# Optimization experiments

Measured on AMD Instinct MI355X. Metric: run time of the kernel, lower is better.

The kernel has to match this reference:

```python
import jax, jax.numpy as jnp
import numpy as np
import itertools

EPSILON = 1e-6
OUT_SIZE = 4096
IN_SIZE = 4096
RANK = 2  # in_rank + len(out_shape)
REGION = np.array([16.0, 16.0], dtype=np.float32)
PRIMES = np.array([2, 3], dtype=np.int64)  # first RANK primes from the buffer
# floor/ceil combinations, same order as itertools.product([True, False], repeat=RANK)
FLOOR_MASK = np.array([[int(b) for b in bools] for bools in itertools.product([True, False], repeat=RANK)], dtype=bool)  # (2**RANK, RANK)


def generate_integer_tuples(means, rr_u, g_u, rng_sizes, region):
    # means: (b, k, RANK); rr_u/g_u: uniform(0,1) samples (b, k, radd/gadd, RANK)
    b, k, rank = means.shape
    m = jax.lax.stop_gradient(means)  # torch uses means.data
    mexp = m[:, :, None, :]
    # all floor/ceil corner combinations of the continuous index tuple
    neigh = jnp.where(FLOOR_MASK[None, None, :, :], jnp.floor(mexp), jnp.ceil(mexp)).astype(jnp.int64)
    # uniform samples over the whole index space
    g_ints = jnp.floor(g_u * (1.0 - EPSILON) * rng_sizes).astype(jnp.int64)
    # uniform samples from a small window around round(means)
    mr = jnp.round(mexp)
    lower = mr - region * 0.5
    upper = mr + region * 0.5
    lower = jnp.where(lower < 0.0, 0.0, lower)
    lower = jnp.where(upper > rng_sizes, rng_sizes - region, lower)
    rr_ints = (rr_u * (1.0 - EPSILON) * region + lower).astype(jnp.int64)
    ints = jnp.concatenate([neigh, g_ints, rr_ints], axis=2)  # (b, k, 2**RANK+gadd+radd, RANK)
    return ints.reshape(b, -1, rank)


def duplicates(tuples):
    # tuples: (b, n, r) int64 -> bool mask (b, n) marking all-but-first occurrences
    b, n, r = tuples.shape
    unique = jnp.prod((tuples + 1) ** PRIMES[:r], axis=2)  # prime-power hash
    sort_idx = jnp.argsort(unique, axis=1)
    sorted_v = jnp.take_along_axis(unique, sort_idx, axis=1)
    unsort_idx = jnp.argsort(sort_idx, axis=1)
    mask = jnp.concatenate(
        [jnp.zeros((b, 1), dtype=bool), sorted_v[:, 1:] == sorted_v[:, :-1]], axis=1)
    return jnp.take_along_axis(mask, unsort_idx, axis=1)


def densities(points, means, sigmas):
    # unnormalized diagonal-MVN pdf: exp(-0.5 * sum_r (p_r - m_r)^2 / (eps + sigma_r))
    # expanded quadratic form via einsum to avoid the (b, n, k, r) intermediate
    inv = 1.0 / (EPSILON + sigmas)                                   # (b, k, r)
    a = jnp.einsum('bnr,bkr->bnk', points * points, inv)
    bt = jnp.einsum('bnr,bkr->bnk', points, means * inv)
    c = jnp.sum(means * means * inv, axis=-1)[:, None, :]
    return jnp.exp(-0.5 * (a - 2.0 * bt + c))                        # (b, n, k)


def setup_inputs() -> dict:
    key = jax.random.key(0)
    ks = jax.random.split(key, 7)
    b, k, gadd, radd = 4, 256, 64, 64
    rng = jnp.array([OUT_SIZE, IN_SIZE], dtype=jnp.float32)
    x = jax.random.normal(ks[0], (b, IN_SIZE), dtype=jnp.float32)
    means = jax.random.uniform(ks[1], (b, k, RANK), dtype=jnp.float32) * (rng - 1.0)
    sigmas = (jax.random.uniform(ks[2], (b, k, RANK), dtype=jnp.float32) * 2.0 + 0.5) * (rng / 64.0)
    values = jax.random.normal(ks[3], (b, k), dtype=jnp.float32)
    bias = jax.random.normal(ks[4], (OUT_SIZE,), dtype=jnp.float32)
    rr_u = jax.random.uniform(ks[5], (b, k, radd, RANK), dtype=jnp.float32)
    g_u = jax.random.uniform(ks[6], (b, k, gadd, RANK), dtype=jnp.float32)
    return {"x": x, "means": means, "sigmas": sigmas, "values": values,
            "bias": bias, "rr_u": rr_u, "g_u": g_u}


def reference(x, means, sigmas, values, bias, rr_u, g_u):
    b, in_size = x.shape
    rng_sizes = jnp.array([OUT_SIZE, in_size], dtype=jnp.float32)
    region = jnp.asarray(REGION)
    indices = jax.lax.stop_gradient(
        generate_integer_tuples(means, rr_u, g_u, rng_sizes, region))  # (b, n, 2)
    dups = duplicates(indices)                                        # (b, n) bool
    props = densities(indices.astype(jnp.float32), means, sigmas)     # (b, n, k)
    props = jnp.where(dups[:, :, None], 0.0, props)                   # zero duplicates
    props = props / props.sum(axis=1, keepdims=True)
    weights = jnp.einsum('bnk,bk->bn', props, values)                 # per-index weight
    out_idx = indices[:, :, 0]  # output coordinate (len(out_shape)=1)
    in_idx = indices[:, :, 1]   # input coordinate (in_rank=1)
    gathered = jnp.take_along_axis(x, in_idx, axis=1)                 # (b, n)
    barange = jnp.arange(b)[:, None]
    y = jnp.zeros((b, OUT_SIZE), dtype=x.dtype).at[barange, out_idx].add(weights * gathered)
    return y + bias[None, :]
```

## Files before the change

### kernel.cpp

```cpp
#include <hip/hip_runtime.h>
#include <cstdint>

#define BATCH 4
#define KCOMP 256
#define GADD 64
#define RADD 64
#define PPK 132
#define NPB (KCOMP * PPK)
#define NTOT (BATCH * NPB)
#define OUTS 4096
#define INS 4096
#define TBITS 16
#define TSIZE (1 << TBITS)
#define TILE 128
#define TILES (NPB / TILE)

#define KEYS_BYTES  ((size_t)BATCH * TSIZE * 8)
#define DENOM_BYTES ((size_t)BATCH * KCOMP * 4)
#define VALS_BYTES  ((size_t)BATCH * TSIZE * 4)
#define PTS_BYTES   ((size_t)NTOT * 4)

#define ZERO_U4 131328
#define FF_U4   65536
#define Y_F4    4096
#define INIT_TOT (ZERO_U4 + FF_U4 + Y_F4)

__device__ __forceinline__ unsigned long long point_hash(long long t0, long long t1) {
    unsigned long long a = (unsigned long long)((t0 + 1) * (t0 + 1));
    unsigned long long b = (unsigned long long)((t1 + 1) * (t1 + 1) * (t1 + 1));
    return a * b;
}

__device__ __forceinline__ unsigned int slot_of(unsigned long long h) {
    return (unsigned int)((h * 0x9E3779B97F4A7C15ull) >> (64 - TBITS));
}

__global__ void k_init(const float* __restrict__ bias, float* __restrict__ y,
                       uint4* __restrict__ zero_base, uint4* __restrict__ ff_base) {
    int i = blockIdx.x * blockDim.x + threadIdx.x;
    if (i < ZERO_U4) {
        zero_base[i] = make_uint4(0u, 0u, 0u, 0u);
    } else if (i < ZERO_U4 + FF_U4) {
        ff_base[i - ZERO_U4] = make_uint4(~0u, ~0u, ~0u, ~0u);
    } else if (i < INIT_TOT) {
        int j = i - (ZERO_U4 + FF_U4);
        float4 bv = ((const float4*)bias)[j & 1023];
        ((float4*)y)[j] = bv;
    }
}

__global__ void k_gen(const float* __restrict__ means,
                      const float* __restrict__ rr_u,
                      const float* __restrict__ g_u,
                      uint32_t* __restrict__ pts,
                      unsigned long long* __restrict__ keys,
                      unsigned int* __restrict__ vals) {
    int i = blockIdx.x * blockDim.x + threadIdx.x;
    int bk, j;
    long long t0, t1;
    if (i < 4096) {
        bk = i >> 2;
        j = i & 3;
        double m0 = (double)means[bk * 2], m1 = (double)means[bk * 2 + 1];
        t0 = (long long)((j < 2) ? floor(m0) : ceil(m0));
        t1 = (long long)(((j & 1) == 0) ? floor(m1) : ceil(m1));
    } else if (i < 4096 + 65536) {
        int i2 = i - 4096;
        bk = i2 >> 6;
        j = 4 + (i2 & 63);
        const float* gp = g_u + (size_t)i2 * 2;
        t0 = (long long)floor((double)gp[0] * (1.0 - 1e-6) * 4096.0);
        t1 = (long long)floor((double)gp[1] * (1.0 - 1e-6) * 4096.0);
    } else {
        int i3 = i - (4096 + 65536);
        bk = i3 >> 6;
        j = 68 + (i3 & 63);
        const float* rp = rr_u + (size_t)i3 * 2;
        double m0 = (double)means[bk * 2], m1 = (double)means[bk * 2 + 1];
        double mr0 = rint(m0), mr1 = rint(m1);
        double lo0 = mr0 - 8.0;
        if (lo0 < 0.0) lo0 = 0.0;
        if (mr0 + 8.0 > 4096.0) lo0 = 4080.0;
        double lo1 = mr1 - 8.0;
        if (lo1 < 0.0) lo1 = 0.0;
        if (mr1 + 8.0 > 4096.0) lo1 = 4080.0;
        t0 = (long long)((double)rp[0] * (1.0 - 1e-6) * 16.0 + lo0);
        t1 = (long long)((double)rp[1] * (1.0 - 1e-6) * 16.0 + lo1);
    }
    int b = bk >> 8;
    int loc = (bk & 255) * PPK + j;

    pts[(size_t)b * NPB + loc] = (uint32_t)t0 | ((uint32_t)t1 << 12);

    unsigned long long h = point_hash(t0, t1);
    unsigned long long* kb = keys + (size_t)b * TSIZE;
    unsigned int* vb = vals + (size_t)b * TSIZE;
    unsigned int s = slot_of(h);
    for (;;) {
        unsigned long long prev = atomicCAS(&kb[s], 0ull, h);
        if (prev == 0ull || prev == h) {
            atomicMin(&vb[s], (unsigned int)loc);
            break;
        }
        s = (s + 1) & (TSIZE - 1);
    }
}

__global__ void k_denomA(const float* __restrict__ means,
                         const float* __restrict__ sigmas,
                         uint32_t* __restrict__ pts,
                         const unsigned long long* __restrict__ keys,
                         const unsigned int* __restrict__ vals,
                         float* __restrict__ denom) {
    __shared__ float2 spt[TILE];
    int bid = blockIdx.x;
    int b = bid / TILES;
    int tile = bid - b * TILES;
    int t = threadIdx.x;

    if (t < TILE) {
        int loc = tile * TILE + t;
        uint32_t p = pts[(size_t)b * NPB + loc];
        long long t0 = (long long)(p & 0xFFFu);
        long long t1 = (long long)((p >> 12) & 0xFFFu);
        unsigned long long h = point_hash(t0, t1);
        const unsigned long long* kb = keys + (size_t)b * TSIZE;
        const unsigned int* vb = vals + (size_t)b * TSIZE;
        unsigned int s = slot_of(h);
        while (kb[s] != h) s = (s + 1) & (TSIZE - 1);
        if (vb[s] != (unsigned int)loc) {
            pts[(size_t)b * NPB + loc] = p | 0x80000000u;
            spt[t] = make_float2(1.0e9f, 0.0f);
        } else {
            spt[t] = make_float2((float)t0, (float)t1);
        }
    }
    __syncthreads();

    int bk = b * KCOMP + t;
    float m0 = means[bk * 2], m1 = means[bk * 2 + 1];
    float i0 = -0.5f / (1e-6f + sigmas[bk * 2]);
    float i1 = -0.5f / (1e-6f + sigmas[bk * 2 + 1]);

    float a0 = 0.f, a1 = 0.f, a2 = 0.f, a3 = 0.f, a4 = 0.f, a5 = 0.f, a6 = 0.f, a7 = 0.f;
#pragma unroll 4
    for (int j = 0; j < TILE; j += 8) {
        float2 q0 = spt[j],     q1 = spt[j + 1], q2 = spt[j + 2], q3 = spt[j + 3];
        float2 q4 = spt[j + 4], q5 = spt[j + 5], q6 = spt[j + 6], q7 = spt[j + 7];
        float dx, dy;
        dx = q0.x - m0; dy = q0.y - m1; a0 += __expf(dx * dx * i0 + dy * dy * i1);
        dx = q1.x - m0; dy = q1.y - m1; a1 += __expf(dx * dx * i0 + dy * dy * i1);
        dx = q2.x - m0; dy = q2.y - m1; a2 += __expf(dx * dx * i0 + dy * dy * i1);
        dx = q3.x - m0; dy = q3.y - m1; a3 += __expf(dx * dx * i0 + dy * dy * i1);
        dx = q4.x - m0; dy = q4.y - m1; a4 += __expf(dx * dx * i0 + dy * dy * i1);
        dx = q5.x - m0; dy = q5.y - m1; a5 += __expf(dx * dx * i0 + dy * dy * i1);
        dx = q6.x - m0; dy = q6.y - m1; a6 += __expf(dx * dx * i0 + dy * dy * i1);
        dx = q7.x - m0; dy = q7.y - m1; a7 += __expf(dx * dx * i0 + dy * dy * i1);
    }
    atomicAdd(&denom[bk], ((a0 + a1) + (a2 + a3)) + ((a4 + a5) + (a6 + a7)));
}

__global__ void k_scatterB(const float* __restrict__ means,
                           const float* __restrict__ sigmas,
                           const float* __restrict__ values,
                           const float* __restrict__ denom,
                           const float* __restrict__ x,
                           const uint32_t* __restrict__ pts,
                           float* __restrict__ y) {
    __shared__ float4 prm[KCOMP];
    __shared__ float cf[KCOMP];
    __shared__ float wpart[TILE];
    int bid = blockIdx.x;
    int b = bid / TILES;
    int tile = bid - b * TILES;
    int t = threadIdx.x;

    {
        int bk = b * KCOMP + t;
        float i0 = -0.5f / (1e-6f + sigmas[bk * 2]);
        float i1 = -0.5f / (1e-6f + sigmas[bk * 2 + 1]);
        prm[t] = make_float4(means[bk * 2], means[bk * 2 + 1], i0, i1);
        cf[t] = values[bk] / denom[bk];
    }
    __syncthreads();

    int pt_i = t & (TILE - 1);
    int kbase = (t >> 7) * 128;
    int loc = tile * TILE + pt_i;
    uint32_t p = pts[(size_t)b * NPB + loc];
    bool live = !(p & 0x80000000u);

    float w = 0.0f;
    if (live) {
        float p0 = (float)(p & 0xFFFu);
        float p1 = (float)((p >> 12) & 0xFFFu);
        float w0 = 0.f, w1 = 0.f, w2 = 0.f, w3 = 0.f, w4 = 0.f, w5 = 0.f, w6 = 0.f, w7 = 0.f;
#pragma unroll 4
        for (int q = kbase; q < kbase + 128; q += 8) {
            float4 r0 = prm[q],     r1 = prm[q + 1], r2 = prm[q + 2], r3 = prm[q + 3];
            float4 r4 = prm[q + 4], r5 = prm[q + 5], r6 = prm[q + 6], r7 = prm[q + 7];
            float dx, dy;
            dx = p0 - r0.x; dy = p1 - r0.y;
            w0 = fmaf(__expf(dx * dx * r0.z + dy * dy * r0.w), cf[q],     w0);
            dx = p0 - r1.x; dy = p1 - r1.y;
            w1 = fmaf(__expf(dx * dx * r1.z + dy * dy * r1.w), cf[q + 1], w1);
            dx = p0 - r2.x; dy = p1 - r2.y;
            w2 = fmaf(__expf(dx * dx * r2.z + dy * dy * r2.w), cf[q + 2], w2);
            dx = p0 - r3.x; dy = p1 - r3.y;
            w3 = fmaf(__expf(dx * dx * r3.z + dy * dy * r3.w), cf[q + 3], w3);
            dx = p0 - r4.x; dy = p1 - r4.y;
            w4 = fmaf(__expf(dx * dx * r4.z + dy * dy * r4.w), cf[q + 4], w4);
            dx = p0 - r5.x; dy = p1 - r5.y;
            w5 = fmaf(__expf(dx * dx * r5.z + dy * dy * r5.w), cf[q + 5], w5);
            dx = p0 - r6.x; dy = p1 - r6.y;
            w6 = fmaf(__expf(dx * dx * r6.z + dy * dy * r6.w), cf[q + 6], w6);
            dx = p0 - r7.x; dy = p1 - r7.y;
            w7 = fmaf(__expf(dx * dx * r7.z + dy * dy * r7.w), cf[q + 7], w7);
        }
        w = ((w0 + w1) + (w2 + w3)) + ((w4 + w5) + (w6 + w7));
    }
    if (t >= TILE) wpart[pt_i] = w;
    __syncthreads();
    if (t < TILE && live) {
        w += wpart[pt_i];
        int out_idx = (int)(p & 0xFFFu);
        int in_idx = (int)((p >> 12) & 0xFFFu);
        atomicAdd(&y[(size_t)b * OUTS + out_idx], w * x[(size_t)b * INS + in_idx]);
    }
}

extern "C" void kernel_launch(void* const* d_in, const int* in_sizes, int n_in,
                              void* d_out, int out_size, void* d_ws, size_t ws_size,
                              hipStream_t stream) {
    const float* x      = (const float*)d_in[0];
    const float* means  = (const float*)d_in[1];
    const float* sigmas = (const float*)d_in[2];
    const float* values = (const float*)d_in[3];
    const float* bias   = (const float*)d_in[4];
    const float* rr_u   = (const float*)d_in[5];
    const float* g_u    = (const float*)d_in[6];
    float* y = (float*)d_out;

    uint8_t* w = (uint8_t*)d_ws;
    unsigned long long* keys = (unsigned long long*)w;
    float* denom = (float*)(w + KEYS_BYTES);
    unsigned int* vals = (unsigned int*)(w + KEYS_BYTES + DENOM_BYTES);
    uint32_t* pts = (uint32_t*)(w + KEYS_BYTES + DENOM_BYTES + VALS_BYTES);

    hipLaunchKernelGGL(k_init, dim3((INIT_TOT + 255) / 256), dim3(256), 0, stream,
                       bias, y, (uint4*)w, (uint4*)(w + KEYS_BYTES + DENOM_BYTES));
    hipLaunchKernelGGL(k_gen, dim3((NTOT + 255) / 256), dim3(256), 0, stream,
                       means, rr_u, g_u, pts, keys, vals);
    hipLaunchKernelGGL(k_denomA, dim3(BATCH * TILES), dim3(256), 0, stream,
                       means, sigmas, pts, keys, vals, denom);
    hipLaunchKernelGGL(k_scatterB, dim3(BATCH * TILES), dim3(256), 0, stream,
                       means, sigmas, values, denom, x, pts, y);
}
```

Before: 132.1 us.

## Fuse four pipeline kernels into one cooperative persistent kernel with grid syncs

Combines init, point generation/hashing, denominator and scatter stages into a single cooperative kernel that loops over work with grid-stride loops, separated by grid.sync(). Grid size is taken from the occupancy query (per-CU blocks × 256, capped at 1024), and the original four-launch path is kept as a fallback. The aim is to remove the launch overhead and inter-kernel gaps between the four small kernels. In exchange it pays for grid-wide barriers, and the capped persistent grid may underuse the GPU compared with the original per-tile launches.

```diff
diff --git a/kernel.cpp b/kernel.cpp
--- a/kernel.cpp
+++ b/kernel.cpp
@@ -1,5 +1,8 @@
 #include <hip/hip_runtime.h>
+#include <hip/hip_cooperative_groups.h>
 #include <cstdint>
+
+namespace cg = cooperative_groups;
 
 #define BATCH 4
 #define KCOMP 256
@@ -14,6 +17,7 @@
 #define TSIZE (1 << TBITS)
 #define TILE 128
 #define TILES (NPB / TILE)
+#define MAX_COOP_BLOCKS 1024
 
 #define KEYS_BYTES  ((size_t)BATCH * TSIZE * 8)
 #define DENOM_BYTES ((size_t)BATCH * KCOMP * 4)
@@ -35,27 +39,12 @@
     return (unsigned int)((h * 0x9E3779B97F4A7C15ull) >> (64 - TBITS));
 }
 
-__global__ void k_init(const float* __restrict__ bias, float* __restrict__ y,
-                       uint4* __restrict__ zero_base, uint4* __restrict__ ff_base) {
-    int i = blockIdx.x * blockDim.x + threadIdx.x;
-    if (i < ZERO_U4) {
-        zero_base[i] = make_uint4(0u, 0u, 0u, 0u);
-    } else if (i < ZERO_U4 + FF_U4) {
-        ff_base[i - ZERO_U4] = make_uint4(~0u, ~0u, ~0u, ~0u);
-    } else if (i < INIT_TOT) {
-        int j = i - (ZERO_U4 + FF_U4);
-        float4 bv = ((const float4*)bias)[j & 1023];
-        ((float4*)y)[j] = bv;
-    }
-}
-
-__global__ void k_gen(const float* __restrict__ means,
-                      const float* __restrict__ rr_u,
-                      const float* __restrict__ g_u,
-                      uint32_t* __restrict__ pts,
-                      unsigned long long* __restrict__ keys,
-                      unsigned int* __restrict__ vals) {
-    int i = blockIdx.x * blockDim.x + threadIdx.x;
+__device__ __forceinline__ void gen_one(int i, const float* __restrict__ means,
+                                        const float* __restrict__ rr_u,
+                                        const float* __restrict__ g_u,
+                                        uint32_t* __restrict__ pts,
+                                        unsigned long long* __restrict__ keys,
+                                        unsigned int* __restrict__ vals) {
     int bk, j;
     long long t0, t1;
     if (i < 4096) {
@@ -106,18 +95,14 @@
     }
 }
 
-__global__ void k_denomA(const float* __restrict__ means,
-                         const float* __restrict__ sigmas,
-                         uint32_t* __restrict__ pts,
-                         const unsigned long long* __restrict__ keys,
-                         const unsigned int* __restrict__ vals,
-                         float* __restrict__ denom) {
-    __shared__ float2 spt[TILE];
-    int bid = blockIdx.x;
-    int b = bid / TILES;
-    int tile = bid - b * TILES;
-    int t = threadIdx.x;
-
+__device__ __forceinline__ void denom_tile(int b, int tile, int t,
+                                           const float* __restrict__ means,
+                                           const float* __restrict__ sigmas,
+                                           uint32_t* __restrict__ pts,
+                                           const unsigned long long* __restrict__ keys,
+                                           const unsigned int* __restrict__ vals,
+                                           float* __restrict__ denom,
+                                           float2* spt) {
     if (t < TILE) {
         int loc = tile * TILE + t;
         uint32_t p = pts[(size_t)b * NPB + loc];
@@ -160,21 +145,15 @@
     atomicAdd(&denom[bk], ((a0 + a1) + (a2 + a3)) + ((a4 + a5) + (a6 + a7)));
 }
 
-__global__ void k_scatterB(const float* __restrict__ means,
-                           const float* __restrict__ sigmas,
-                           const float* __restrict__ values,
-                           const float* __restrict__ denom,
-                           const float* __restrict__ x,
-                           const uint32_t* __restrict__ pts,
-                           float* __restrict__ y) {
-    __shared__ float4 prm[KCOMP];
-    __shared__ float cf[KCOMP];
-    __shared__ float wpart[TILE];
-    int bid = blockIdx.x;
-    int b = bid / TILES;
-    int tile = bid - b * TILES;
-    int t = threadIdx.x;
-
+__device__ __forceinline__ void scatter_tile(int b, int tile, int t,
+                                             const float* __restrict__ means,
+                                             const float* __restrict__ sigmas,
+                                             const float* __restrict__ values,
+                                             const float* __restrict__ denom,
+                                             const float* __restrict__ x,
+                                             const uint32_t* __restrict__ pts,
+                                             float* __restrict__ y,
+                                             float4* prm, float* cf, float* wpart) {
     {
         int bk = b * KCOMP + t;
         float i0 = -0.5f / (1e-6f + sigmas[bk * 2]);
@@ -229,6 +208,96 @@
     }
 }
 
+__global__ __launch_bounds__(256, 4)
+void k_fused(const float* __restrict__ x, const float* __restrict__ means,
+             const float* __restrict__ sigmas, const float* __restrict__ values,
+             const float* __restrict__ bias, const float* __restrict__ rr_u,
+             const float* __restrict__ g_u, float* __restrict__ y,
+             unsigned long long* __restrict__ keys, unsigned int* __restrict__ vals,
+             uint32_t* __restrict__ pts, float* __restrict__ denom) {
+    cg::grid_group grid = cg::this_grid();
+    const int t = threadIdx.x;
+    const int nb = gridDim.x;
+    const int stride = nb * 256;
+    const int gtid0 = blockIdx.x * 256 + t;
+
+    __shared__ float2 spt[TILE];
+    __shared__ float4 prm[KCOMP];
+    __shared__ float cf[KCOMP];
+    __shared__ float wpart[TILE];
+
+    for (int i = gtid0; i < INIT_TOT; i += stride) {
+        if (i < ZERO_U4) {
+            ((uint4*)keys)[i] = make_uint4(0u, 0u, 0u, 0u);
+        } else if (i < ZERO_U4 + FF_U4) {
+            ((uint4*)vals)[i - ZERO_U4] = make_uint4(~0u, ~0u, ~0u, ~0u);
+        } else {
+            int j = i - (ZERO_U4 + FF_U4);
+            ((float4*)y)[j] = ((const float4*)bias)[j & 1023];
+        }
+    }
+    grid.sync();
+
+    for (int i = gtid0; i < NTOT; i += stride)
+        gen_one(i, means, rr_u, g_u, pts, keys, vals);
+    grid.sync();
+
+    for (int tt = blockIdx.x; tt < BATCH * TILES; tt += nb) {
+        denom_tile(tt / TILES, tt % TILES, t, means, sigmas, pts, keys, vals,
+                   denom, spt);
+        __syncthreads();
+    }
+    grid.sync();
+
+    for (int tt = blockIdx.x; tt < BATCH * TILES; tt += nb) {
+        scatter_tile(tt / TILES, tt % TILES, t, means, sigmas, values, denom,
+                     x, pts, y, prm, cf, wpart);
+        __syncthreads();
+    }
+}
+
+__global__ void k_init(const float* __restrict__ bias, float* __restrict__ y,
+                       uint4* __restrict__ zero_base, uint4* __restrict__ ff_base) {
+    int i = blockIdx.x * blockDim.x + threadIdx.x;
+    if (i < ZERO_U4) {
+        zero_base[i] = make_uint4(0u, 0u, 0u, 0u);
+    } else if (i < ZERO_U4 + FF_U4) {
+        ff_base[i - ZERO_U4] = make_uint4(~0u, ~0u, ~0u, ~0u);
+    } else if (i < INIT_TOT) {
+        int j = i - (ZERO_U4 + FF_U4);
+        ((float4*)y)[j] = ((const float4*)bias)[j & 1023];
+    }
+}
+
+__global__ void k_gen(const float* __restrict__ means, const float* __restrict__ rr_u,
+                      const float* __restrict__ g_u, uint32_t* __restrict__ pts,
+                      unsigned long long* __restrict__ keys,
+                      unsigned int* __restrict__ vals) {
+    int i = blockIdx.x * blockDim.x + threadIdx.x;
+    if (i < NTOT) gen_one(i, means, rr_u, g_u, pts, keys, vals);
+}
+
+__global__ void k_denomA(const float* __restrict__ means, const float* __restrict__ sigmas,
+                         uint32_t* __restrict__ pts,
+                         const unsigned long long* __restrict__ keys,
+                         const unsigned int* __restrict__ vals,
+                         float* __restrict__ denom) {
+    __shared__ float2 spt[TILE];
+    denom_tile(blockIdx.x / TILES, blockIdx.x % TILES, threadIdx.x,
+               means, sigmas, pts, keys, vals, denom, spt);
+}
+
+__global__ void k_scatterB(const float* __restrict__ means, const float* __restrict__ sigmas,
+                           const float* __restrict__ values, const float* __restrict__ denom,
+                           const float* __restrict__ x, const uint32_t* __restrict__ pts,
+                           float* __restrict__ y) {
+    __shared__ float4 prm[KCOMP];
+    __shared__ float cf[KCOMP];
+    __shared__ float wpart[TILE];
+    scatter_tile(blockIdx.x / TILES, blockIdx.x % TILES, threadIdx.x,
+                 means, sigmas, values, denom, x, pts, y, prm, cf, wpart);
+}
+
 extern "C" void kernel_launch(void* const* d_in, const int* in_sizes, int n_in,
                               void* d_out, int out_size, void* d_ws, size_t ws_size,
                               hipStream_t stream) {
@@ -247,12 +316,29 @@
     unsigned int* vals = (unsigned int*)(w + KEYS_BYTES + DENOM_BYTES);
     uint32_t* pts = (uint32_t*)(w + KEYS_BYTES + DENOM_BYTES + VALS_BYTES);
 
-    hipLaunchKernelGGL(k_init, dim3((INIT_TOT + 255) / 256), dim3(256), 0, stream,
-                       bias, y, (uint4*)w, (uint4*)(w + KEYS_BYTES + DENOM_BYTES));
-    hipLaunchKernelGGL(k_gen, dim3((NTOT + 255) / 256), dim3(256), 0, stream,
-                       means, rr_u, g_u, pts, keys, vals);
-    hipLaunchKernelGGL(k_denomA, dim3(BATCH * TILES), dim3(256), 0, stream,
-                       means, sigmas, pts, keys, vals, denom);
-    hipLaunchKernelGGL(k_scatterB, dim3(BATCH * TILES), dim3(256), 0, stream,
-                       means, sigmas, values, denom, x, pts, y);
-}
+    int per_cu = 0;
+    hipError_t qerr = hipOccupancyMaxActiveBlocksPerMultiprocessor(
+        &per_cu, (const void*)k_fused, 256, 0);
+    bool coop_done = false;
+    if (qerr == hipSuccess && per_cu >= 1) {
+        int grid = per_cu * 256;
+        if (grid > MAX_COOP_BLOCKS) grid = MAX_COOP_BLOCKS;
+        void* args[] = { (void*)&x, (void*)&means, (void*)&sigmas, (void*)&values,
+                         (void*)&bias, (void*)&rr_u, (void*)&g_u, (void*)&y,
+                         (void*)&keys, (void*)&vals, (void*)&pts, (void*)&denom };
+        hipError_t lerr = hipLaunchCooperativeKernel((const void*)k_fused,
+                                                     dim3(grid), dim3(256),
+                                                     args, 0, stream);
+        coop_done = (lerr == hipSuccess);
+    }
+    if (!coop_done) {
+        hipLaunchKernelGGL(k_init, dim3((INIT_TOT + 255) / 256), dim3(256), 0, stream,
+                           bias, y, (uint4*)w, (uint4*)(w + KEYS_BYTES + DENOM_BYTES));
+        hipLaunchKernelGGL(k_gen, dim3((NTOT + 255) / 256), dim3(256), 0, stream,
+                           means, rr_u, g_u, pts, keys, vals);
+        hipLaunchKernelGGL(k_denomA, dim3(BATCH * TILES), dim3(256), 0, stream,
+                           means, sigmas, pts, keys, vals, denom);
+        hipLaunchKernelGGL(k_scatterB, dim3(BATCH * TILES), dim3(256), 0, stream,
+                           means, sigmas, values, denom, x, pts, y);
+    }
+}
```

Measured after the change: 288.8 us. 119% more time.
